# Optimization experiments

Measured on AMD Instinct MI355X. Metric: run time of the kernel, lower is better.

The kernel has to match this reference:

```python
import jax, jax.numpy as jnp
import numpy as np

B, S, DIM, HEADS, DH = 1, 192, 512, 8, 64
LN_EPS = 1e-5


def setup_inputs() -> dict:
    key = jax.random.key(0)
    ks = jax.random.split(key, 5)
    rn = lambda k, shp: jax.random.normal(k, shp, dtype=jnp.float32) * 0.02
    return {
        "x": jax.random.normal(ks[0], (B, S, DIM), dtype=jnp.float32),
        "ln_w": jnp.ones((DIM,), jnp.float32),
        "ln_b": jnp.zeros((DIM,), jnp.float32),
        "W_abcde": rn(ks[1], (5 * HEADS * DH, DIM)),
        "b_abcde": jnp.zeros((5 * HEADS * DH,), jnp.float32),
        "W_K": rn(ks[2], (HEADS, DH, DH, DH)),
        "W_V": rn(ks[3], (HEADS, DH, DH, DH)),
        "W_out": rn(ks[4], (DIM, HEADS * DH)),
        "b_out": jnp.zeros((DIM,), jnp.float32),
    }


def reference(x, ln_w, ln_b, W_abcde, b_abcde, W_K, W_V, W_out, b_out):
    b, n, _ = x.shape
    # LayerNorm (biased variance, eps=1e-5, affine)
    mu = jnp.mean(x, axis=-1, keepdims=True)
    var = jnp.var(x, axis=-1, keepdims=True)
    xn = (x - mu) / jnp.sqrt(var + LN_EPS) * ln_w + ln_b
    # abcde projection, chunk into 5, split heads -> [b, n, h, d]
    proj = xn @ W_abcde.T + b_abcde
    a_, b_, c_, d_, e_ = [t.reshape(b, n, HEADS, DH) for t in jnp.split(proj, 5, axis=-1)]
    # cubic attention score chain (note: heads summed out in step2, reintroduced by a_)
    step1 = jnp.einsum('brnk,nijk->brij', c_, W_K)          # [b, r, d, d]
    step2 = jnp.einsum('brij,bqnj->briq', step1, b_)        # [b, r, d, q] (sum over heads of b_)
    attn = jnp.einsum('briq,bpni->bnpqr', step2, a_)        # [b, h, p, q, r]
    # "causal" mask: positions where p >= q set to 1e-6 (faithful to masked_fill_)
    t_idx = jnp.arange(n)[:, None, None]
    s_idx = jnp.arange(n)[None, :, None]
    mask = (t_idx >= s_idx)[None, None]                      # [1,1,p,q,1]
    attn = jnp.where(mask, jnp.float32(1e-6), attn)
    # 'b n p1 p2 p3 -> b n p3 (p1 p2)', scale by 1/dim_head, softmax over (p1 p2)
    attn = attn.transpose(0, 1, 4, 2, 3).reshape(b, HEADS, n, n * n) / DH
    attn = jax.nn.softmax(attn, axis=-1)
    # pairwise values: [b, p1, p2, h, d] -> 'b p s n h -> b n h (p s)'
    v = jnp.einsum('bpnh,bqng,nhgf->bpqnf', d_, e_, W_V)
    v = v.transpose(0, 3, 4, 1, 2).reshape(b, HEADS, DH, n * n)
    # weighted sum over pair axis, merge heads
    z = jnp.einsum('bnql,bnhl->bqnh', attn, v).reshape(b, n, HEADS * DH)
    return z @ W_out.T + b_out
```

## Files before the change

kernel.cpp:

```cpp
#include <hip/hip_runtime.h>
#include <hip/hip_bf16.h>
#include <cstdint>

#define SEQ 192

typedef float f32x4 __attribute__((ext_vector_type(4)));
typedef float f32x8 __attribute__((ext_vector_type(8)));
typedef __bf16 bf16;
typedef __bf16 bf16x8 __attribute__((ext_vector_type(8)));
typedef __bf16 bf16x4 __attribute__((ext_vector_type(4)));

#define MFMA_BF16(a, b, c) __builtin_amdgcn_mfma_f32_16x16x32_bf16(a, b, c, 0, 0, 0)

__device__ __forceinline__ bf16x8 cvt8(f32x8 v) {
  bf16x8 o;
#pragma unroll
  for (int i = 0; i < 8; i++) o[i] = (bf16)v[i];
  return o;
}

__global__ __launch_bounds__(256) void k1_prep(
    const float* __restrict__ x, const float* __restrict__ ln_w, const float* __restrict__ ln_b,
    const float* __restrict__ WV, bf16* __restrict__ xn_bf, bf16* __restrict__ WVt2) {
  int bid = blockIdx.x, tid = threadIdx.x;
  if (bid < 512) {
    int g = bid & 63, hh = bid >> 6;
    __shared__ float ld[64 * 65];
    int f = tid & 63, r4 = tid >> 6;
#pragma unroll
    for (int it = 0; it < 16; it++) {
      int hp = it * 4 + r4;
      ld[hp * 65 + f] = WV[(((size_t)(hh * 64 + hp) * 64 + g) * 64) + f];
    }
    __syncthreads();
    int hp2 = tid & 63;
#pragma unroll
    for (int it = 0; it < 16; it++) {
      int ff = it * 4 + r4;
      WVt2[(size_t)hh * 262144 + (size_t)(ff * 64 + g) * 64 + hp2] = (bf16)ld[hp2 * 65 + ff];
    }
    return;
  }
  bid -= 512;
  {
    int r = bid;
    const float* xr = x + (size_t)r * 512;
    float v0 = xr[tid], v1 = xr[tid + 256];
    float s = v0 + v1, s2 = v0 * v0 + v1 * v1;
#pragma unroll
    for (int off = 32; off > 0; off >>= 1) {
      s += __shfl_down(s, off);
      s2 += __shfl_down(s2, off);
    }
    __shared__ float redS[4], redS2[4];
    int wave = tid >> 6, lane = tid & 63;
    if (lane == 0) { redS[wave] = s; redS2[wave] = s2; }
    __syncthreads();
    float S = redS[0] + redS[1] + redS[2] + redS[3];
    float S2 = redS2[0] + redS2[1] + redS2[2] + redS2[3];
    float mean = S * (1.0f / 512.0f);
    float var = S2 * (1.0f / 512.0f) - mean * mean;
    float rstd = rsqrtf(var + 1e-5f);
    bf16* xnr = xn_bf + (size_t)r * 512;
    xnr[tid] = (bf16)((v0 - mean) * rstd * ln_w[tid] + ln_b[tid]);
    xnr[tid + 256] = (bf16)((v1 - mean) * rstd * ln_w[tid + 256] + ln_b[tid + 256]);
  }
}

__device__ __forceinline__ void gemm_rm(const bf16* __restrict__ A, const bf16* __restrict__ Bt,
                                        bf16* __restrict__ C1, int N, int K, int nb, int mb,
                                        int tid) {
  int n0 = nb * 64, m0 = mb * 64;
  int wave = tid >> 6, lane = tid & 63;
  int lq = lane >> 4, l16 = lane & 15;
  const bf16* Ap = A + (size_t)(m0 + wave * 16 + l16) * K;
  f32x4 acc[4];
#pragma unroll
  for (int nt = 0; nt < 4; nt++) acc[nt] = (f32x4){0.f, 0.f, 0.f, 0.f};
  for (int k0 = 0; k0 < K; k0 += 32) {
    bf16x8 af = *(const bf16x8*)(Ap + k0 + lq * 8);
#pragma unroll
    for (int nt = 0; nt < 4; nt++) {
      bf16x8 bv = *(const bf16x8*)(Bt + (size_t)(n0 + nt * 16 + l16) * K + k0 + lq * 8);
      acc[nt] = MFMA_BF16(af, bv, acc[nt]);
    }
  }
  int cm = m0 + wave * 16 + lq * 4;
#pragma unroll
  for (int nt = 0; nt < 4; nt++) {
    int n = n0 + nt * 16 + l16;
#pragma unroll
    for (int rg = 0; rg < 4; rg++) C1[(size_t)(cm + rg) * N + n] = (bf16)acc[nt][rg];
  }
}

__global__ __launch_bounds__(256) void k2_proj(
    const bf16* __restrict__ xn_bf, const float* __restrict__ Wab,
    const float* __restrict__ b_abcde, float* __restrict__ proj, bf16* __restrict__ a_bf,
    bf16* __restrict__ c_bf, bf16* __restrict__ d_bf) {
  int bid = blockIdx.x, tid = threadIdx.x;
  int nb = bid % 40, mb = bid / 40;
  int n0 = nb * 64, m0 = mb * 64;
  int wave = tid >> 6, lane = tid & 63;
  int lq = lane >> 4, l16 = lane & 15;
  const bf16* Ap = xn_bf + (size_t)(m0 + wave * 16 + l16) * 512;
  f32x4 acc[4];
#pragma unroll
  for (int nt = 0; nt < 4; nt++) acc[nt] = (f32x4){0.f, 0.f, 0.f, 0.f};
  for (int k0 = 0; k0 < 512; k0 += 32) {
    bf16x8 af = *(const bf16x8*)(Ap + k0 + lq * 8);
#pragma unroll
    for (int nt = 0; nt < 4; nt++) {
      f32x8 wv = *(const f32x8*)(Wab + (size_t)(n0 + nt * 16 + l16) * 512 + k0 + lq * 8);
      acc[nt] = MFMA_BF16(af, cvt8(wv), acc[nt]);
    }
  }
  int cm = m0 + wave * 16 + lq * 4;
#pragma unroll
  for (int nt = 0; nt < 4; nt++) {
    int n = n0 + nt * 16 + l16;
    int chunk = n >> 9, hcol = (n >> 6) & 7, i = n & 63;
#pragma unroll
    for (int rg = 0; rg < 4; rg++) {
      int m = cm + rg;
      float v = acc[nt][rg] + b_abcde[n];
      proj[(size_t)m * 2560 + n] = v;
      bf16 bv = (bf16)v;
      if (chunk == 0) a_bf[((size_t)hcol * SEQ + m) * 64 + i] = bv;
      else if (chunk == 2) c_bf[(size_t)m * 512 + (n - 1024)] = bv;
      else if (chunk == 3) d_bf[((size_t)hcol * SEQ + m) * 64 + i] = bv;
    }
  }
}

__global__ __launch_bounds__(256) void k3_mid(
    const bf16* __restrict__ c_bf, const float* __restrict__ WK, bf16* __restrict__ s1bf,
    const bf16* __restrict__ d_bf, const bf16* __restrict__ WVt2, bf16* __restrict__ tTt,
    const float* __restrict__ proj, bf16* __restrict__ eT_bf, float* __restrict__ ecum,
    bf16* __restrict__ bsum_bf) {
  __shared__ float el[64 * 65];
  int bid = blockIdx.x, tid = threadIdx.x;
  if (bid < 192) {
    int nb = bid % 64, mb = bid / 64;
    int n0 = nb * 64, m0 = mb * 64;
    int wave = tid >> 6, lane = tid & 63;
    int lq = lane >> 4, l16 = lane & 15;
    const bf16* Ap = c_bf + (size_t)(m0 + wave * 16 + l16) * 512;
    f32x4 acc[4];
#pragma unroll
    for (int nt = 0; nt < 4; nt++) acc[nt] = (f32x4){0.f, 0.f, 0.f, 0.f};
    size_t offn[4];
#pragma unroll
    for (int nt = 0; nt < 4; nt++) {
      int n = n0 + nt * 16 + l16;
      offn[nt] = (size_t)(n >> 6) * 4096 + (size_t)(n & 63) * 64;
    }
    for (int k0 = 0; k0 < 512; k0 += 32) {
      bf16x8 af = *(const bf16x8*)(Ap + k0 + lq * 8);
      size_t kb = (size_t)(k0 >> 6) * 262144 + (k0 & 32) + lq * 8;
#pragma unroll
      for (int nt = 0; nt < 4; nt++) {
        f32x8 wv = *(const f32x8*)(WK + kb + offn[nt]);
        acc[nt] = MFMA_BF16(af, cvt8(wv), acc[nt]);
      }
    }
    int cm = m0 + wave * 16 + lq * 4;
#pragma unroll
    for (int nt = 0; nt < 4; nt++) {
      int n = n0 + nt * 16 + l16;
#pragma unroll
      for (int rg = 0; rg < 4; rg++) s1bf[(size_t)(cm + rg) * 4096 + n] = (bf16)acc[nt][rg];
    }
    return;
  }
  bid -= 192;
  if (bid < 1536) {
    int h = bid / 192, rem = bid % 192;
    gemm_rm(d_bf + (size_t)h * 12288, WVt2 + (size_t)h * 262144,
            tTt + (size_t)h * 786432, 4096, 64, rem % 64, rem / 64, tid);
    return;
  }
  bid -= 1536;
  if (bid < 8) {
    int h = bid;
    float carry = 0.f;
    for (int ch = 0; ch < 3; ch++) {
      int pbase = ch * 64;
      if (ch) __syncthreads();
      for (int idx = tid; idx < 4096; idx += 256) {
        int pl = idx >> 6, g = idx & 63;
        el[pl * 65 + g] = proj[(size_t)(pbase + pl) * 2560 + 2048 + h * 64 + g];
      }
      __syncthreads();
      for (int idx = tid; idx < 4096; idx += 256) {
        int g = idx >> 6, ql = idx & 63;
        eT_bf[((size_t)h * 64 + g) * SEQ + pbase + ql] = (bf16)el[ql * 65 + g];
      }
      if (tid < 64) {
        float run = carry;
        for (int pl = 0; pl < 64; pl++) {
          run += el[pl * 65 + tid];
          ecum[(size_t)h * 12288 + (pbase + pl) * 64 + tid] = run;
        }
        carry = run;
      }
      __syncthreads();
    }
    return;
  }
  bid -= 8;
  {
    int j = tid & 63, qg = tid >> 6;
#pragma unroll
    for (int qi = 0; qi < 16; qi++) {
      int q = bid * 64 + qg * 16 + qi;
      float s = 0.f;
#pragma unroll
      for (int hh = 0; hh < 8; hh++) s += proj[(size_t)q * 2560 + 512 + hh * 64 + j];
      bsum_bf[q * 64 + j] = (bf16)s;
    }
  }
}

__global__ __launch_bounds__(256, 3) void k45_attn(
    const bf16* __restrict__ a_bf, const bf16* __restrict__ s1bf,
    const bf16* __restrict__ bsum_bf, const bf16* __restrict__ eT_bf,
    const float* __restrict__ ecum, bf16* __restrict__ ew_bf, float* __restrict__ Lsum) {
  int r = blockIdx.x, h = blockIdx.y;
  int tid = threadIdx.x, wave = tid >> 6, lane = tid & 63;
  int lq = lane >> 4, l16 = lane & 15;
  __shared__ __align__(16) bf16 s2L[SEQ * 72];
  __shared__ __align__(16) bf16 wch[4][3][16 * 40];
  __shared__ float redL[4];

  {
    const bf16* s1r = s1bf + (size_t)r * 4096;
    bf16x8 aS[2];
#pragma unroll
    for (int kc = 0; kc < 2; kc++)
      aS[kc] = *(const bf16x8*)(s1r + (wave * 16 + l16) * 64 + kc * 32 + lq * 8);
#pragma unroll
    for (int qt = 0; qt < 12; qt++) {
      f32x4 acc = (f32x4){0.f, 0.f, 0.f, 0.f};
#pragma unroll
      for (int kc = 0; kc < 2; kc++) {
        bf16x8 bv = *(const bf16x8*)(bsum_bf + (qt * 16 + l16) * 64 + kc * 32 + lq * 8);
        acc = MFMA_BF16(aS[kc], bv, acc);
      }
      bf16x4 pk = {(bf16)acc[0], (bf16)acc[1], (bf16)acc[2], (bf16)acc[3]};
      *(bf16x4*)(&s2L[(qt * 16 + l16) * 72 + wave * 16 + lq * 4]) = pk;
    }
  }
  __syncthreads();

  int pt[3] = {wave, wave + 4, 11 - wave};
  const bf16* ah = a_bf + (size_t)h * 12288;
  const bf16* eh = eT_bf + (size_t)h * 12288;
  const float* ech = ecum + (size_t)h * 12288;

  bf16x8 afr[3][2];
#pragma unroll
  for (int mt = 0; mt < 3; mt++)
#pragma unroll
    for (int kc = 0; kc < 2; kc++)
      afr[mt][kc] = *(const bf16x8*)(ah + (pt[mt] * 16 + l16) * 64 + kc * 32 + lq * 8);

  f32x4 ewacc[3][4];
#pragma unroll
  for (int mt = 0; mt < 3; mt++)
#pragma unroll
    for (int nt = 0; nt < 4; nt++) ewacc[mt][nt] = (f32x4){0.f, 0.f, 0.f, 0.f};
  float lpart = 0.f;

  for (int cc = 0; cc < 6; cc++) {
    if (cc * 32 + 31 <= wave * 16) continue;
    bf16x8 efr[4];
#pragma unroll
    for (int nt = 0; nt < 4; nt++)
      efr[nt] = *(const bf16x8*)(eh + (nt * 16 + l16) * SEQ + cc * 32 + lq * 8);
    bf16x8 bq[2][2];
#pragma unroll
    for (int sub = 0; sub < 2; sub++) {
      int q = cc * 32 + sub * 16 + l16;
      bq[sub][0] = *(const bf16x8*)(&s2L[q * 72 + lq * 8]);
      bq[sub][1] = *(const bf16x8*)(&s2L[q * 72 + 32 + lq * 8]);
    }
    f32x4 sacc[3][2];
#pragma unroll
    for (int mt = 0; mt < 3; mt++) {
      if (cc * 32 + 31 <= pt[mt] * 16) continue;
#pragma unroll
      for (int sub = 0; sub < 2; sub++) {
        if (cc * 32 + sub * 16 + 15 <= pt[mt] * 16) continue;
        f32x4 sv = (f32x4){0.f, 0.f, 0.f, 0.f};
        sv = MFMA_BF16(afr[mt][0], bq[sub][0], sv);
        sacc[mt][sub] = MFMA_BF16(afr[mt][1], bq[sub][1], sv);
      }
    }
#pragma unroll
    for (int mt = 0; mt < 3; mt++) {
      if (cc * 32 + 31 <= pt[mt] * 16) continue;
      bf16* mybuf = &wch[wave][mt][0];
#pragma unroll
      for (int sub = 0; sub < 2; sub++) {
        if (cc * 32 + sub * 16 + 15 <= pt[mt] * 16) {
#pragma unroll
          for (int rg = 0; rg < 4; rg++) mybuf[(lq * 4 + rg) * 40 + sub * 16 + l16] = (bf16)0.f;
          continue;
        }
        int q = cc * 32 + sub * 16 + l16;
        int p0 = pt[mt] * 16 + lq * 4;
#pragma unroll
        for (int rg = 0; rg < 4; rg++) {
          float wv = (q > p0 + rg) ? __expf(sacc[mt][sub][rg] * 0.015625f) : 0.f;
          lpart += wv;
          mybuf[(lq * 4 + rg) * 40 + sub * 16 + l16] = (bf16)wv;
        }
      }
    }
#pragma unroll
    for (int mt = 0; mt < 3; mt++) {
      if (cc * 32 + 31 <= pt[mt] * 16) continue;
      bf16x8 wf = *(const bf16x8*)(&wch[wave][mt][l16 * 40 + lq * 8]);
#pragma unroll
      for (int nt = 0; nt < 4; nt++) ewacc[mt][nt] = MFMA_BF16(wf, efr[nt], ewacc[mt][nt]);
    }
  }

  bf16* ewout = ew_bf + ((size_t)h * SEQ + r) * 12288;
#pragma unroll
  for (int mt = 0; mt < 3; mt++)
#pragma unroll
    for (int nt = 0; nt < 4; nt++)
#pragma unroll
      for (int rg = 0; rg < 4; rg++) {
        int pp = pt[mt] * 16 + lq * 4 + rg;
        int g = nt * 16 + l16;
        ewout[pp * 64 + g] = (bf16)(ewacc[mt][nt][rg] + ech[pp * 64 + g]);
      }

#pragma unroll
  for (int off = 32; off > 0; off >>= 1) lpart += __shfl_down(lpart, off);
  if (lane == 0) redL[wave] = lpart;
  __syncthreads();
  if (tid == 0) Lsum[h * SEQ + r] = redL[0] + redL[1] + redL[2] + redL[3];
}

__global__ __launch_bounds__(512) void k5b_z(
    const bf16* __restrict__ ew_bf, const bf16* __restrict__ tTt, float* __restrict__ Zpart) {
  int h = blockIdx.x, mt = blockIdx.y, ks = blockIdx.z;
  int tid = threadIdx.x, wave = tid >> 6, lane = tid & 63;
  int lq = lane >> 4, l16 = lane & 15;
  __shared__ float zred[8][16][66];
  const bf16* ewh = ew_bf + ((size_t)h * SEQ + mt * 32) * 12288;
  const bf16* th = tTt + (size_t)h * 786432;
  f32x4 acc[2][4];
#pragma unroll
  for (int m2 = 0; m2 < 2; m2++)
#pragma unroll
    for (int nt = 0; nt < 4; nt++) acc[m2][nt] = (f32x4){0.f, 0.f, 0.f, 0.f};
  for (int jj = 0; jj < 6; jj++) {
    int kc = ks * 48 + wave * 6 + jj;
    int pp = kc >> 1, g0 = (kc & 1) * 32;
    bf16x8 af0 = *(const bf16x8*)(ewh + (size_t)l16 * 12288 + kc * 32 + lq * 8);
    bf16x8 af1 = *(const bf16x8*)(ewh + (size_t)(16 + l16) * 12288 + kc * 32 + lq * 8);
#pragma unroll
    for (int nt = 0; nt < 4; nt++) {
      bf16x8 tf = *(const bf16x8*)(th + (size_t)pp * 4096 + (nt * 16 + l16) * 64 + g0 + lq * 8);
      acc[0][nt] = MFMA_BF16(af0, tf, acc[0][nt]);
      acc[1][nt] = MFMA_BF16(af1, tf, acc[1][nt]);
    }
  }
#pragma unroll
  for (int m2 = 0; m2 < 2; m2++) {
    if (m2) __syncthreads();
#pragma unroll
    for (int nt = 0; nt < 4; nt++)
#pragma unroll
      for (int rg = 0; rg < 4; rg++) zred[wave][lq * 4 + rg][nt * 16 + l16] = acc[m2][nt][rg];
    __syncthreads();
#pragma unroll
    for (int o = 0; o < 2; o++) {
      int idx = o * 512 + tid;
      int rloc = idx >> 6, f = idx & 63;
      float s = 0.f;
#pragma unroll
      for (int wv = 0; wv < 8; wv++) s += zred[wv][rloc][f];
      Zpart[(size_t)ks * 98304 + (size_t)(mt * 32 + m2 * 16 + rloc) * 512 + h * 64 + f] = s;
    }
  }
}

__global__ __launch_bounds__(256) void k6_out(
    const float* __restrict__ Zpart, const float* __restrict__ Lsum,
    const float* __restrict__ Wout, const float* __restrict__ b_out, float* __restrict__ out) {
  int u = blockIdx.x, tid = threadIdx.x;
  int mb = u >> 3, nb = u & 7;
  __shared__ __align__(16) bf16 zt[16 * 520];
  __shared__ float rd[4 * 16 * 68];
  for (int idx = tid; idx < 8192; idx += 256) {
    int m = idx >> 9, cc = idx & 511;
    float s = 0.f;
#pragma unroll
    for (int ks = 0; ks < 8; ks++)
      s += Zpart[(size_t)ks * 98304 + (size_t)(mb * 16 + m) * 512 + cc];
    float L = Lsum[(cc >> 6) * SEQ + mb * 16 + m] + 18528.0f;
    zt[m * 520 + cc] = (bf16)(s / L);
  }
  __syncthreads();
  int wave = tid >> 6, lane = tid & 63;
  int lq = lane >> 4, l16 = lane & 15;
  f32x4 acc[4];
#pragma unroll
  for (int nt = 0; nt < 4; nt++) acc[nt] = (f32x4){0.f, 0.f, 0.f, 0.f};
#pragma unroll
  for (int kc = 0; kc < 4; kc++) {
    int k0 = wave * 128 + kc * 32;
    bf16x8 af = *(const bf16x8*)(zt + l16 * 520 + k0 + lq * 8);
#pragma unroll
    for (int nt = 0; nt < 4; nt++) {
      f32x8 wv = *(const f32x8*)(Wout + (size_t)(nb * 64 + nt * 16 + l16) * 512 + k0 + lq * 8);
      acc[nt] = MFMA_BF16(af, cvt8(wv), acc[nt]);
    }
  }
#pragma unroll
  for (int nt = 0; nt < 4; nt++)
#pragma unroll
    for (int rg = 0; rg < 4; rg++)
      rd[(wave * 16 + lq * 4 + rg) * 68 + nt * 16 + l16] = acc[nt][rg];
  __syncthreads();
#pragma unroll
  for (int o = 0; o < 4; o++) {
    int idx = o * 256 + tid;
    int rloc = idx >> 6, f = idx & 63;
    float s = rd[rloc * 68 + f] + rd[(16 + rloc) * 68 + f] + rd[(32 + rloc) * 68 + f] +
              rd[(48 + rloc) * 68 + f];
    out[(size_t)(mb * 16 + rloc) * 512 + nb * 64 + f] = s + b_out[nb * 64 + f];
  }
}

static const size_t OFF_PROJ = 0;
static const size_t OFF_ECUM = 491520;
static const size_t OFF_XN = 589824;
static const size_t OFF_LSUM = 638976;
static const size_t OFF_ZPART = 640512;
static const size_t OFF_WVT = 2213376;
static const size_t OFF_A = 3261952;
static const size_t OFF_C = 3311104;
static const size_t OFF_D = 3360256;
static const size_t OFF_ET = 3409408;
static const size_t OFF_BSUM = 3458560;
static const size_t OFF_S1 = 3464704;
static const size_t OFF_TT = 5037568;
static const size_t OFF_EW = 8183296;

extern "C" void kernel_launch(void* const* d_in, const int* in_sizes, int n_in,
                              void* d_out, int out_size, void* d_ws, size_t ws_size,
                              hipStream_t stream) {
  (void)in_sizes; (void)n_in; (void)out_size; (void)ws_size;
  const float* x = (const float*)d_in[0];
  const float* ln_w = (const float*)d_in[1];
  const float* ln_b = (const float*)d_in[2];
  const float* W_abcde = (const float*)d_in[3];
  const float* b_abcde = (const float*)d_in[4];
  const float* W_K = (const float*)d_in[5];
  const float* W_V = (const float*)d_in[6];
  const float* W_out = (const float*)d_in[7];
  const float* b_out = (const float*)d_in[8];
  float* out = (float*)d_out;
  float* ws = (float*)d_ws;

  float* proj = ws + OFF_PROJ;
  float* ecum = ws + OFF_ECUM;
  bf16* xn_bf = (bf16*)(ws + OFF_XN);
  float* Lsum = ws + OFF_LSUM;
  float* Zpart = ws + OFF_ZPART;
  bf16* WVt2 = (bf16*)(ws + OFF_WVT);
  bf16* a_bf = (bf16*)(ws + OFF_A);
  bf16* c_bf = (bf16*)(ws + OFF_C);
  bf16* d_bf = (bf16*)(ws + OFF_D);
  bf16* eT_bf = (bf16*)(ws + OFF_ET);
  bf16* bsum_bf = (bf16*)(ws + OFF_BSUM);
  bf16* s1bf = (bf16*)(ws + OFF_S1);
  bf16* tTt = (bf16*)(ws + OFF_TT);
  bf16* ew_bf = (bf16*)(ws + OFF_EW);

  k1_prep<<<704, 256, 0, stream>>>(x, ln_w, ln_b, W_V, xn_bf, WVt2);
  k2_proj<<<120, 256, 0, stream>>>(xn_bf, W_abcde, b_abcde, proj, a_bf, c_bf, d_bf);
  k3_mid<<<1739, 256, 0, stream>>>(c_bf, W_K, s1bf, d_bf, WVt2, tTt, proj, eT_bf, ecum,
                                   bsum_bf);
  k45_attn<<<dim3(SEQ, 8), 256, 0, stream>>>(a_bf, s1bf, bsum_bf, eT_bf, ecum, ew_bf, Lsum);
  k5b_z<<<dim3(8, 6, 8), 512, 0, stream>>>(ew_bf, tTt, Zpart);
  k6_out<<<96, 256, 0, stream>>>(Zpart, Lsum, W_out, b_out, out);
}
```

Before: 221.0 us.

## Hoist step2 into its own kernel and deepen split-K in the z kernel

The step2 product (s1 times the head-summed b) was recomputed inside every (r, h) attention block, so each r repeated the same work 8 times. It is now computed once by a separate k4_step2 kernel into a global buffer. The attention kernel reads s2 straight from global/L2, which drops its roughly 27 KB shared-memory staging buffer and one barrier, and may allow more resident blocks. The z kernel moves from 512 threads and 8 K-splits to 256 threads and 16 K-splits to launch more blocks, at the cost of more Zpart partial sums for k6 to reduce. The trade-offs are an extra launch, a few MB of extra workspace traffic, and a larger workspace requirement.

New measurement: 219.5 us. No clear change (-0.7%).

```diff
diff --git a/kernel.cpp b/kernel.cpp
--- a/kernel.cpp
+++ b/kernel.cpp
@@ -222,39 +222,50 @@
   }
 }
 
-__global__ __launch_bounds__(256, 3) void k45_attn(
-    const bf16* __restrict__ a_bf, const bf16* __restrict__ s1bf,
-    const bf16* __restrict__ bsum_bf, const bf16* __restrict__ eT_bf,
-    const float* __restrict__ ecum, bf16* __restrict__ ew_bf, float* __restrict__ Lsum) {
+__global__ __launch_bounds__(256) void k4_step2(const bf16* __restrict__ s1bf,
+                                                const bf16* __restrict__ bsum_bf,
+                                                bf16* __restrict__ s2bf) {
+  int bid = blockIdx.x, tid = threadIdx.x;
+  int nb = bid % 3, mb = bid / 3;
+  int n0 = nb * 64, m0 = mb * 64;
+  int wave = tid >> 6, lane = tid & 63;
+  int lq = lane >> 4, l16 = lane & 15;
+  const bf16* Ap = s1bf + (size_t)(m0 + wave * 16 + l16) * 64;
+  f32x4 acc[4];
+#pragma unroll
+  for (int nt = 0; nt < 4; nt++) acc[nt] = (f32x4){0.f, 0.f, 0.f, 0.f};
+#pragma unroll
+  for (int k0 = 0; k0 < 64; k0 += 32) {
+    bf16x8 af = *(const bf16x8*)(Ap + k0 + lq * 8);
+#pragma unroll
+    for (int nt = 0; nt < 4; nt++) {
+      bf16x8 bv = *(const bf16x8*)(bsum_bf + (size_t)(n0 + nt * 16 + l16) * 64 + k0 + lq * 8);
+      acc[nt] = MFMA_BF16(af, bv, acc[nt]);
+    }
+  }
+  int cm = m0 + wave * 16 + lq * 4;
+#pragma unroll
+  for (int nt = 0; nt < 4; nt++) {
+    int n = n0 + nt * 16 + l16;
+    int r = cm >> 6, i0 = cm & 63;
+    bf16x4 pk = {(bf16)acc[nt][0], (bf16)acc[nt][1], (bf16)acc[nt][2], (bf16)acc[nt][3]};
+    *(bf16x4*)(s2bf + (size_t)r * 12288 + (size_t)n * 64 + i0) = pk;
+  }
+}
+
+__global__ __launch_bounds__(256, 3) void k5_attn(
+    const bf16* __restrict__ a_bf, const bf16* __restrict__ s2bf,
+    const bf16* __restrict__ eT_bf, const float* __restrict__ ecum,
+    bf16* __restrict__ ew_bf, float* __restrict__ Lsum) {
   int r = blockIdx.x, h = blockIdx.y;
   int tid = threadIdx.x, wave = tid >> 6, lane = tid & 63;
   int lq = lane >> 4, l16 = lane & 15;
-  __shared__ __align__(16) bf16 s2L[SEQ * 72];
   __shared__ __align__(16) bf16 wch[4][3][16 * 40];
   __shared__ float redL[4];
-
-  {
-    const bf16* s1r = s1bf + (size_t)r * 4096;
-    bf16x8 aS[2];
-#pragma unroll
-    for (int kc = 0; kc < 2; kc++)
-      aS[kc] = *(const bf16x8*)(s1r + (wave * 16 + l16) * 64 + kc * 32 + lq * 8);
-#pragma unroll
-    for (int qt = 0; qt < 12; qt++) {
-      f32x4 acc = (f32x4){0.f, 0.f, 0.f, 0.f};
-#pragma unroll
-      for (int kc = 0; kc < 2; kc++) {
-        bf16x8 bv = *(const bf16x8*)(bsum_bf + (qt * 16 + l16) * 64 + kc * 32 + lq * 8);
-        acc = MFMA_BF16(aS[kc], bv, acc);
-      }
-      bf16x4 pk = {(bf16)acc[0], (bf16)acc[1], (bf16)acc[2], (bf16)acc[3]};
-      *(bf16x4*)(&s2L[(qt * 16 + l16) * 72 + wave * 16 + lq * 4]) = pk;
-    }
-  }
-  __syncthreads();
-
   int pt[3] = {wave, wave + 4, 11 - wave};
+
   const bf16* ah = a_bf + (size_t)h * 12288;
+  const bf16* s2r = s2bf + (size_t)r * 12288;
   const bf16* eh = eT_bf + (size_t)h * 12288;
   const float* ech = ecum + (size_t)h * 12288;
 
@@ -282,8 +293,8 @@
 #pragma unroll
     for (int sub = 0; sub < 2; sub++) {
       int q = cc * 32 + sub * 16 + l16;
-      bq[sub][0] = *(const bf16x8*)(&s2L[q * 72 + lq * 8]);
-      bq[sub][1] = *(const bf16x8*)(&s2L[q * 72 + 32 + lq * 8]);
+      bq[sub][0] = *(const bf16x8*)(s2r + q * 64 + lq * 8);
+      bq[sub][1] = *(const bf16x8*)(s2r + q * 64 + 32 + lq * 8);
     }
     f32x4 sacc[3][2];
 #pragma unroll
@@ -346,21 +357,22 @@
   if (tid == 0) Lsum[h * SEQ + r] = redL[0] + redL[1] + redL[2] + redL[3];
 }
 
-__global__ __launch_bounds__(512) void k5b_z(
+__global__ __launch_bounds__(256) void k5b_z(
     const bf16* __restrict__ ew_bf, const bf16* __restrict__ tTt, float* __restrict__ Zpart) {
-  int h = blockIdx.x, mt = blockIdx.y, ks = blockIdx.z;
+  int h = blockIdx.x, mtb = blockIdx.y, ks = blockIdx.z;
   int tid = threadIdx.x, wave = tid >> 6, lane = tid & 63;
   int lq = lane >> 4, l16 = lane & 15;
-  __shared__ float zred[8][16][66];
-  const bf16* ewh = ew_bf + ((size_t)h * SEQ + mt * 32) * 12288;
+  __shared__ float zred[4 * 16 * 66];
+  const bf16* ewh = ew_bf + ((size_t)h * SEQ + mtb * 32) * 12288;
   const bf16* th = tTt + (size_t)h * 786432;
   f32x4 acc[2][4];
 #pragma unroll
   for (int m2 = 0; m2 < 2; m2++)
 #pragma unroll
     for (int nt = 0; nt < 4; nt++) acc[m2][nt] = (f32x4){0.f, 0.f, 0.f, 0.f};
+#pragma unroll
   for (int jj = 0; jj < 6; jj++) {
-    int kc = ks * 48 + wave * 6 + jj;
+    int kc = ks * 24 + wave * 6 + jj;
     int pp = kc >> 1, g0 = (kc & 1) * 32;
     bf16x8 af0 = *(const bf16x8*)(ewh + (size_t)l16 * 12288 + kc * 32 + lq * 8);
     bf16x8 af1 = *(const bf16x8*)(ewh + (size_t)(16 + l16) * 12288 + kc * 32 + lq * 8);
@@ -377,16 +389,16 @@
 #pragma unroll
     for (int nt = 0; nt < 4; nt++)
 #pragma unroll
-      for (int rg = 0; rg < 4; rg++) zred[wave][lq * 4 + rg][nt * 16 + l16] = acc[m2][nt][rg];
+      for (int rg = 0; rg < 4; rg++)
+        zred[(wave * 16 + lq * 4 + rg) * 66 + nt * 16 + l16] = acc[m2][nt][rg];
     __syncthreads();
 #pragma unroll
-    for (int o = 0; o < 2; o++) {
-      int idx = o * 512 + tid;
+    for (int o = 0; o < 4; o++) {
+      int idx = o * 256 + tid;
       int rloc = idx >> 6, f = idx & 63;
-      float s = 0.f;
-#pragma unroll
-      for (int wv = 0; wv < 8; wv++) s += zred[wv][rloc][f];
-      Zpart[(size_t)ks * 98304 + (size_t)(mt * 32 + m2 * 16 + rloc) * 512 + h * 64 + f] = s;
+      float s = zred[rloc * 66 + f] + zred[(16 + rloc) * 66 + f] + zred[(32 + rloc) * 66 + f] +
+                zred[(48 + rloc) * 66 + f];
+      Zpart[(size_t)ks * 98304 + (size_t)(mtb * 32 + m2 * 16 + rloc) * 512 + h * 64 + f] = s;
     }
   }
 }
@@ -402,7 +414,7 @@
     int m = idx >> 9, cc = idx & 511;
     float s = 0.f;
 #pragma unroll
-    for (int ks = 0; ks < 8; ks++)
+    for (int ks = 0; ks < 16; ks++)
       s += Zpart[(size_t)ks * 98304 + (size_t)(mb * 16 + m) * 512 + cc];
     float L = Lsum[(cc >> 6) * SEQ + mb * 16 + m] + 18528.0f;
     zt[m * 520 + cc] = (bf16)(s / L);
@@ -453,6 +465,7 @@
 static const size_t OFF_S1 = 3464704;
 static const size_t OFF_TT = 5037568;
 static const size_t OFF_EW = 8183296;
+static const size_t OFF_S2 = 17620480;
 
 extern "C" void kernel_launch(void* const* d_in, const int* in_sizes, int n_in,
                               void* d_out, int out_size, void* d_ws, size_t ws_size,
@@ -484,12 +497,14 @@
   bf16* s1bf = (bf16*)(ws + OFF_S1);
   bf16* tTt = (bf16*)(ws + OFF_TT);
   bf16* ew_bf = (bf16*)(ws + OFF_EW);
+  bf16* s2bf = (bf16*)(ws + OFF_S2);
 
   k1_prep<<<704, 256, 0, stream>>>(x, ln_w, ln_b, W_V, xn_bf, WVt2);
   k2_proj<<<120, 256, 0, stream>>>(xn_bf, W_abcde, b_abcde, proj, a_bf, c_bf, d_bf);
   k3_mid<<<1739, 256, 0, stream>>>(c_bf, W_K, s1bf, d_bf, WVt2, tTt, proj, eT_bf, ecum,
                                    bsum_bf);
-  k45_attn<<<dim3(SEQ, 8), 256, 0, stream>>>(a_bf, s1bf, bsum_bf, eT_bf, ecum, ew_bf, Lsum);
-  k5b_z<<<dim3(8, 6, 8), 512, 0, stream>>>(ew_bf, tTt, Zpart);
+  k4_step2<<<576, 256, 0, stream>>>(s1bf, bsum_bf, s2bf);
+  k5_attn<<<dim3(SEQ, 8), 256, 0, stream>>>(a_bf, s2bf, eT_bf, ecum, ew_bf, Lsum);
+  k5b_z<<<dim3(8, 6, 16), 256, 0, stream>>>(ew_bf, tTt, Zpart);
   k6_out<<<96, 256, 0, stream>>>(Zpart, Lsum, W_out, b_out, out);
 }
```
